# Performance work log

Measured on AMD Instinct MI355X. Metric: run time of the kernel, lower is better.

Reference implementation:

```python
import jax, jax.numpy as jnp
import numpy as np

E, D, H = 8, 512, 2048  # num_experts, features, features*mlp_ratio
B, S = 4, 512


def _lecun(key, shape):
    fan_in = shape[-2] if len(shape) >= 2 else shape[0]
    return jax.random.normal(key, shape, dtype=jnp.float32) / jnp.sqrt(jnp.float32(fan_in))


def setup_inputs() -> dict:
    key = jax.random.key(0)
    ks = jax.random.split(key, 8)
    return {
        'x_real': jax.random.normal(ks[0], (B, S, D), dtype=jnp.float32),
        'x_imag': jax.random.normal(ks[1], (B, S, D), dtype=jnp.float32),
        # gating Dense over concat([amp, phase]) -> in_features = 2*D
        'gate_W': _lecun(ks[2], (2 * D, E)),
        'gate_b': jnp.zeros((E,), jnp.float32),
        # per-expert ComplexLinear 1: D -> H
        'W1r': _lecun(ks[3], (E, D, H)),
        'W1i': _lecun(ks[4], (E, D, H)),
        'b1r': jnp.zeros((E, H), jnp.float32),
        'b1i': jnp.zeros((E, H), jnp.float32),
        # per-expert ComplexModReLU bias
        'mod_b': jnp.zeros((E, H), jnp.float32),
        # per-expert ComplexLinear 2: H -> D
        'W2r': _lecun(ks[5], (E, H, D)),
        'W2i': _lecun(ks[6], (E, H, D)),
        'b2r': jnp.zeros((E, D), jnp.float32),
        'b2i': jnp.zeros((E, D), jnp.float32),
    }


def reference(x_real, x_imag, gate_W, gate_b, W1r, W1i, b1r, b1i, mod_b, W2r, W2i, b2r, b2i):
    eps = 1e-10
    # --- gating: scores over [|z|, angle(z)] ---
    amp = jnp.sqrt(x_real ** 2 + x_imag ** 2)            # |z|, [B,S,D]
    phase = jnp.arctan2(x_imag, x_real)                  # angle(z)
    routing_input = jnp.concatenate([amp, phase], axis=-1)  # [B,S,2D]
    scores = routing_input @ gate_W + gate_b             # [B,S,E]
    probs = jax.nn.softmax(scores, axis=-1)
    idx = jnp.argmax(probs, axis=-1)                     # [B,S] top-1 expert

    # --- all experts dense (faithful to reference): complex linear 1 ---
    # (Wr + iWi)(xr + ixi) : hr = xr Wr - xi Wi ; hi = xr Wi + xi Wr
    h_r = (jnp.einsum('bsd,edh->ebsh', x_real, W1r)
           - jnp.einsum('bsd,edh->ebsh', x_imag, W1i)) + b1r[:, None, None, :]
    h_i = (jnp.einsum('bsd,edh->ebsh', x_real, W1i)
           + jnp.einsum('bsd,edh->ebsh', x_imag, W1r)) + b1i[:, None, None, :]

    # --- ComplexModReLU: relu(|z|+b) * z / (|z|+eps), |z| = sqrt(r^2+i^2+eps) ---
    a = jnp.sqrt(h_r ** 2 + h_i ** 2 + eps)              # [E,B,S,H]
    scale = jax.nn.relu(a + mod_b[:, None, None, :]) / (a + eps)
    h_r = h_r * scale
    h_i = h_i * scale

    # --- complex linear 2 ---
    o_r = (jnp.einsum('ebsh,ehd->ebsd', h_r, W2r)
           - jnp.einsum('ebsh,ehd->ebsd', h_i, W2i)) + b2r[:, None, None, :]
    o_i = (jnp.einsum('ebsh,ehd->ebsd', h_r, W2i)
           + jnp.einsum('ebsh,ehd->ebsd', h_i, W2r)) + b2i[:, None, None, :]

    # --- mask + weight (top-1): out = sum_e out_e * probs[...,e] * (argmax==e) ---
    e_ids = jnp.arange(probs.shape[-1])
    w = jnp.transpose(probs, (2, 0, 1)) * (idx[None, :, :] == e_ids[:, None, None])  # [E,B,S]
    out_r = jnp.einsum('ebs,ebsd->bsd', w, o_r)
    out_i = jnp.einsum('ebs,ebsd->bsd', w, o_i)
    return (out_r, out_i)
```

## Files before the change

kernel.cpp:

```cpp
#include <hip/hip_runtime.h>
#include <math.h>

#define NE 8
#define ND 512
#define NH 2048
#define NT 2048
#define MAXIT 40

typedef __attribute__((ext_vector_type(8))) short short8;
typedef __attribute__((ext_vector_type(4))) float f32x4;

#define GLL(g, d) __builtin_amdgcn_global_load_lds( \
    (const __attribute__((address_space(1))) void*)(g), \
    (__attribute__((address_space(3))) void*)(d), 16, 0, 0)

__device__ __forceinline__ unsigned short f2bf(float x) {
    unsigned int u = __builtin_bit_cast(unsigned int, x);
    u += 0x7FFFu + ((u >> 16) & 1u);
    return (unsigned short)(u >> 16);
}

__device__ __forceinline__ short8 lds8(const unsigned short* p) {
    return *(const short8*)p;
}

__global__ __launch_bounds__(256) void gate_kernel(
    const float* __restrict__ xr, const float* __restrict__ xi,
    const float* __restrict__ gW, const float* __restrict__ gb,
    float* __restrict__ gate_w,
    int* __restrict__ counts, int* __restrict__ tok_list,
    unsigned short* __restrict__ obr, unsigned short* __restrict__ obi)
{
    int t = blockIdx.x;
    int tid = threadIdx.x;
    const float* xrt = xr + (size_t)t * ND;
    const float* xit = xi + (size_t)t * ND;

    #pragma unroll
    for (int d = tid; d < ND; d += 256) {
        obr[(size_t)t * ND + d] = f2bf(xrt[d]);
        obi[(size_t)t * ND + d] = f2bf(xit[d]);
    }

    float acc[NE] = {0,0,0,0,0,0,0,0};
    for (int r = tid; r < 2 * ND; r += 256) {
        int d = r & (ND - 1);
        float a = xrt[d], b = xit[d];
        float v = (r < ND) ? sqrtf(a * a + b * b) : atan2f(b, a);
        const float4* g = (const float4*)(gW + (size_t)r * NE);
        float4 g0 = g[0], g1 = g[1];
        acc[0] += v * g0.x; acc[1] += v * g0.y; acc[2] += v * g0.z; acc[3] += v * g0.w;
        acc[4] += v * g1.x; acc[5] += v * g1.y; acc[6] += v * g1.z; acc[7] += v * g1.w;
    }
    #pragma unroll
    for (int e = 0; e < NE; e++) {
        for (int off = 32; off > 0; off >>= 1)
            acc[e] += __shfl_down(acc[e], off, 64);
    }
    __shared__ float part[4][NE];
    int wave = tid >> 6, lane = tid & 63;
    if (lane == 0) {
        #pragma unroll
        for (int e = 0; e < NE; e++) part[wave][e] = acc[e];
    }
    __syncthreads();
    if (tid == 0) {
        float s[NE];
        #pragma unroll
        for (int e = 0; e < NE; e++)
            s[e] = part[0][e] + part[1][e] + part[2][e] + part[3][e] + gb[e];
        int amax = 0; float m = s[0];
        #pragma unroll
        for (int e = 1; e < NE; e++) if (s[e] > m) { m = s[e]; amax = e; }
        float denom = 0.f;
        #pragma unroll
        for (int e = 0; e < NE; e++) denom += expf(s[e] - m);
        gate_w[t] = 1.0f / denom;
        int pos = atomicAdd(&counts[amax], 1);
        tok_list[amax * NT + pos] = t;
    }
}

__global__ __launch_bounds__(256) void transw_kernel(
    const float* __restrict__ s0, unsigned short* __restrict__ d0,
    const float* __restrict__ s1, unsigned short* __restrict__ d1,
    int R, int C, int* __restrict__ counts, int zero_counts)
{
    __shared__ unsigned short t[64][72];
    if (zero_counts && blockIdx.x == 0 && blockIdx.y == 0 && blockIdx.z == 0
        && threadIdx.x < 16)
        counts[threadIdx.x] = 0;
    int e = blockIdx.z;
    int c0 = blockIdx.x * 64, r0 = blockIdx.y * 64;
    size_t off = (size_t)e * R * C;
    int tid = threadIdx.x;
    #pragma unroll
    for (int p = 0; p < 2; ++p) {
        const float* src = (p ? s1 : s0) + off;
        unsigned short* dst = (p ? d1 : d0) + off;
        if (p) __syncthreads();
        #pragma unroll
        for (int i = 0; i < 4; ++i) {
            int r = i * 16 + (tid >> 4);
            int c4 = (tid & 15) * 4;
            float4 v = *(const float4*)&src[(size_t)(r0 + r) * C + c0 + c4];
            t[c4 + 0][r] = f2bf(v.x);
            t[c4 + 1][r] = f2bf(v.y);
            t[c4 + 2][r] = f2bf(v.z);
            t[c4 + 3][r] = f2bf(v.w);
        }
        __syncthreads();
        #pragma unroll
        for (int i = 0; i < 2; ++i) {
            int c = i * 32 + (tid >> 3);
            int r8 = (tid & 7) * 8;
            short8 v = *(const short8*)&t[c][r8];
            *(short8*)&dst[(size_t)(c0 + c) * R + r0 + r8] = v;
        }
    }
}


#define STAGE_(SA_R, SA_I, SB_R, SB_I, ko) do {  \
    GLL(gAr0 + (ko), SA_R + (w * 16) * 64);      \
    GLL(gAi0 + (ko), SA_I + (w * 16) * 64);      \
    GLL(gAr1 + (ko), SA_R + (w * 16 + 8) * 64);  \
    GLL(gAi1 + (ko), SA_I + (w * 16 + 8) * 64);  \
    GLL(gBr0 + (ko), SB_R + (w * 16) * 64);      \
    GLL(gBr1 + (ko), SB_R + (w * 16 + 8) * 64);  \
    GLL(gBi0 + (ko), SB_I + (w * 16) * 64);      \
    GLL(gBi1 + (ko), SB_I + (w * 16 + 8) * 64);  \
} while (0)

#define COMPUTE_(SA_R, SA_I, SB_R, SB_I) do {                                          \
    _Pragma("unroll")                                                                  \
    for (int ks = 0; ks < 2; ++ks) {                                                   \
        int pa = ((ks * 4 + quad) ^ (l15 & 7)) * 8;                                    \
        short8 br  = lds8(SB_R + (w * 16 + l15) * 64 + pa);                            \
        short8 bi2 = lds8(SB_I + (w * 16 + l15) * 64 + pa);                            \
        _Pragma("unroll")                                                              \
        for (int m = 0; m < 4; ++m) {                                                  \
            short8 ar  = lds8(SA_R + (m * 16 + l15) * 64 + pa);                        \
            short8 ai2 = lds8(SA_I + (m * 16 + l15) * 64 + pa);                        \
            aRR[m] = __builtin_amdgcn_mfma_f32_16x16x32_bf16(ar,  br,  aRR[m], 0, 0, 0); \
            aII[m] = __builtin_amdgcn_mfma_f32_16x16x32_bf16(ai2, bi2, aII[m], 0, 0, 0); \
            aRI[m] = __builtin_amdgcn_mfma_f32_16x16x32_bf16(ar,  bi2, aRI[m], 0, 0, 0); \
            aIR[m] = __builtin_amdgcn_mfma_f32_16x16x32_bf16(ai2, br,  aIR[m], 0, 0, 0); \
        }                                                                              \
    }                                                                                  \
} while (0)

#define VMW8  asm volatile("s_waitcnt vmcnt(8)" ::: "memory")
#define VMW0  asm volatile("s_waitcnt vmcnt(0)" ::: "memory")
#define BARX do {                            \
    __builtin_amdgcn_sched_barrier(0);       \
    __builtin_amdgcn_s_barrier();            \
    __builtin_amdgcn_sched_barrier(0);       \
} while (0)

#define MOE_LDS_DECL                                                        \
    __shared__ alignas(16) unsigned short sAr0[4096], sAi0[4096];           \
    __shared__ alignas(16) unsigned short sBr0[4096], sBi0[4096];           \
    __shared__ alignas(16) unsigned short sAr1[4096], sAi1[4096];           \
    __shared__ alignas(16) unsigned short sBr1[4096], sBi1[4096];

#define PIPE_LOOP(NK) do {                                                  \
    STAGE_(sAr0, sAi0, sBr0, sBi0, 0);                                      \
    VMW0; BARX;                                                             \
    _Pragma("unroll 1")                                                     \
    for (int kt = 0; kt < (NK); kt += 2) {                                  \
        if (kt + 1 < (NK)) { STAGE_(sAr1, sAi1, sBr1, sBi1, (kt + 1) * 64); VMW8; } \
        else VMW0;                                                          \
        BARX;                                                               \
        __builtin_amdgcn_s_setprio(1);                                      \
        COMPUTE_(sAr0, sAi0, sBr0, sBi0);                                   \
        __builtin_amdgcn_s_setprio(0);                                      \
        BARX;                                                               \
        if (kt + 2 < (NK)) { STAGE_(sAr0, sAi0, sBr0, sBi0, (kt + 2) * 64); VMW8; } \
        else VMW0;                                                          \
        BARX;                                                               \
        __builtin_amdgcn_s_setprio(1);                                      \
        COMPUTE_(sAr1, sAi1, sBr1, sBi1);                                   \
        __builtin_amdgcn_s_setprio(0);                                      \
        BARX;                                                               \
    }                                                                       \
} while (0)

__device__ __forceinline__ bool find_item(const int* counts, int item,
                                          int& e, int& mt, int& n) {
    int rem = item;
    for (e = 0; e < NE; ++e) {
        n = counts[e];
        int m = (n + 63) >> 6;
        if (rem < m) { mt = rem; return true; }
        rem -= m;
    }
    return false;
}

__global__ __launch_bounds__(256, 2) void moe1_kernel(
    const unsigned short* __restrict__ xbr, const unsigned short* __restrict__ xbi,
    const unsigned short* __restrict__ w1tr, const unsigned short* __restrict__ w1ti,
    const float* __restrict__ b1r, const float* __restrict__ b1i,
    const float* __restrict__ mod_b,
    const int* __restrict__ counts, const int* __restrict__ tok_list,
    unsigned short* __restrict__ hr, unsigned short* __restrict__ hi)
{
    int e, mt, n;
    if (!find_item(counts, blockIdx.x >> 5, e, mt, n)) return;
    int nt = blockIdx.x & 31;
    int mbase = mt * 64, n0 = nt * 64;

    int tid = threadIdx.x;
    int w = tid >> 6, l = tid & 63;
    int l15 = l & 15, quad = l >> 4;
    int swz = (((l & 7) ^ ((l >> 3) & 7)) * 8);

    MOE_LDS_DECL

    const int* tl = tok_list + e * NT;
    int ia0 = mbase + w * 16 + (l >> 3);
    int ia1 = ia0 + 8;
    int ra0 = tl[ia0 < n ? ia0 : n - 1];
    int ra1 = tl[ia1 < n ? ia1 : n - 1];
    const unsigned short* gAr0 = xbr + (size_t)ra0 * ND + swz;
    const unsigned short* gAi0 = xbi + (size_t)ra0 * ND + swz;
    const unsigned short* gAr1 = xbr + (size_t)ra1 * ND + swz;
    const unsigned short* gAi1 = xbi + (size_t)ra1 * ND + swz;
    size_t brow = (size_t)e * NH + n0 + w * 16 + (l >> 3);
    const unsigned short* gBr0 = w1tr + brow * ND + swz;
    const unsigned short* gBr1 = w1tr + (brow + 8) * ND + swz;
    const unsigned short* gBi0 = w1ti + brow * ND + swz;
    const unsigned short* gBi1 = w1ti + (brow + 8) * ND + swz;

    f32x4 aRR[4] = {}, aII[4] = {}, aRI[4] = {}, aIR[4] = {};

    PIPE_LOOP(ND / 64);

    int col = n0 + w * 16 + l15;
    float bre = b1r[(size_t)e * NH + col];
    float bie = b1i[(size_t)e * NH + col];
    float mbv = mod_b[(size_t)e * NH + col];
    #pragma unroll
    for (int m = 0; m < 4; ++m) {
        #pragma unroll
        for (int r = 0; r < 4; ++r) {
            int tix = m * 16 + quad * 4 + r;
            if (mbase + tix >= n) continue;
            int tok = tl[mbase + tix];
            float vr = aRR[m][r] - aII[m][r] + bre;
            float vi = aRI[m][r] + aIR[m][r] + bie;
            float a = sqrtf(vr * vr + vi * vi + 1e-10f);
            float sc = fmaxf(a + mbv, 0.0f) / (a + 1e-10f);
            hr[(size_t)tok * NH + col] = f2bf(vr * sc);
            hi[(size_t)tok * NH + col] = f2bf(vi * sc);
        }
    }
}

__global__ __launch_bounds__(256, 2) void moe2_kernel(
    const unsigned short* __restrict__ hr, const unsigned short* __restrict__ hi,
    const unsigned short* __restrict__ w2tr, const unsigned short* __restrict__ w2ti,
    const float* __restrict__ b2r, const float* __restrict__ b2i,
    const int* __restrict__ counts, const int* __restrict__ tok_list,
    const float* __restrict__ gate_w,
    float* __restrict__ out)
{
    int e, mt, n;
    if (!find_item(counts, blockIdx.x >> 3, e, mt, n)) return;
    int nt = blockIdx.x & 7;
    int mbase = mt * 64, n0 = nt * 64;

    int tid = threadIdx.x;
    int w = tid >> 6, l = tid & 63;
    int l15 = l & 15, quad = l >> 4;
    int swz = (((l & 7) ^ ((l >> 3) & 7)) * 8);

    MOE_LDS_DECL

    const int* tl = tok_list + e * NT;
    int ia0 = mbase + w * 16 + (l >> 3);
    int ia1 = ia0 + 8;
    int ra0 = tl[ia0 < n ? ia0 : n - 1];
    int ra1 = tl[ia1 < n ? ia1 : n - 1];
    const unsigned short* gAr0 = hr + (size_t)ra0 * NH + swz;
    const unsigned short* gAi0 = hi + (size_t)ra0 * NH + swz;
    const unsigned short* gAr1 = hr + (size_t)ra1 * NH + swz;
    const unsigned short* gAi1 = hi + (size_t)ra1 * NH + swz;
    size_t brow = (size_t)e * ND + n0 + w * 16 + (l >> 3);
    const unsigned short* gBr0 = w2tr + brow * NH + swz;
    const unsigned short* gBr1 = w2tr + (brow + 8) * NH + swz;
    const unsigned short* gBi0 = w2ti + brow * NH + swz;
    const unsigned short* gBi1 = w2ti + (brow + 8) * NH + swz;

    f32x4 aRR[4] = {}, aII[4] = {}, aRI[4] = {}, aIR[4] = {};

    PIPE_LOOP(NH / 64);

    int col = n0 + w * 16 + l15;
    float bre = b2r[(size_t)e * ND + col];
    float bie = b2i[(size_t)e * ND + col];
    #pragma unroll
    for (int m = 0; m < 4; ++m) {
        #pragma unroll
        for (int r = 0; r < 4; ++r) {
            int tix = m * 16 + quad * 4 + r;
            if (mbase + tix >= n) continue;
            int tok = tl[mbase + tix];
            float gw = gate_w[tok];
            out[(size_t)tok * ND + col] = (aRR[m][r] - aII[m][r] + bre) * gw;
            out[(size_t)NT * ND + (size_t)tok * ND + col] = (aRI[m][r] + aIR[m][r] + bie) * gw;
        }
    }
}

extern "C" void kernel_launch(void* const* d_in, const int* in_sizes, int n_in,
                              void* d_out, int out_size, void* d_ws, size_t ws_size,
                              hipStream_t stream) {
    const float* xr   = (const float*)d_in[0];
    const float* xi   = (const float*)d_in[1];
    const float* gW   = (const float*)d_in[2];
    const float* gb   = (const float*)d_in[3];
    const float* W1r  = (const float*)d_in[4];
    const float* W1i  = (const float*)d_in[5];
    const float* b1r  = (const float*)d_in[6];
    const float* b1i  = (const float*)d_in[7];
    const float* modb = (const float*)d_in[8];
    const float* W2r  = (const float*)d_in[9];
    const float* W2i  = (const float*)d_in[10];
    const float* b2r  = (const float*)d_in[11];
    const float* b2i  = (const float*)d_in[12];
    float* out = (float*)d_out;

    char* ws = (char*)d_ws;
    int*   counts   = (int*)ws;
    float* gate_w   = (float*)(ws + 256);
    int*   tok_list = (int*)(ws + 256 + 8192);
    size_t off = 256 + 8192 + (size_t)NE * NT * 4;
    unsigned short* xbr  = (unsigned short*)(ws + off); off += (size_t)NT * ND * 2;
    unsigned short* xbi  = (unsigned short*)(ws + off); off += (size_t)NT * ND * 2;
    unsigned short* w1tr = (unsigned short*)(ws + off); off += (size_t)NE * ND * NH * 2;
    unsigned short* w1ti = (unsigned short*)(ws + off); off += (size_t)NE * ND * NH * 2;
    unsigned short* w2tr = (unsigned short*)(ws + off); off += (size_t)NE * ND * NH * 2;
    unsigned short* w2ti = (unsigned short*)(ws + off); off += (size_t)NE * ND * NH * 2;
    unsigned short* h_r  = (unsigned short*)(ws + off); off += (size_t)NT * NH * 2;
    unsigned short* h_i  = (unsigned short*)(ws + off); off += (size_t)NT * NH * 2;

    transw_kernel<<<dim3(NH / 64, ND / 64, NE), 256, 0, stream>>>(
        W1r, w1tr, W1i, w1ti, ND, NH, counts, 1);
    transw_kernel<<<dim3(ND / 64, NH / 64, NE), 256, 0, stream>>>(
        W2r, w2tr, W2i, w2ti, NH, ND, counts, 0);
    gate_kernel<<<NT, 256, 0, stream>>>(xr, xi, gW, gb, gate_w, counts, tok_list, xbr, xbi);
    moe1_kernel<<<MAXIT * 32, 256, 0, stream>>>(
        xbr, xbi, w1tr, w1ti, b1r, b1i, modb, counts, tok_list, h_r, h_i);
    moe2_kernel<<<MAXIT * 8, 256, 0, stream>>>(
        h_r, h_i, w2tr, w2ti, b2r, b2i, counts, tok_list, gate_w, out);
}
```

Measured before the change: 297.6 us.

## Use 4-stage LDS ring pipeline, merge weight transposes, remap block-to-tile order

```diff
diff --git a/kernel.cpp b/kernel.cpp
--- a/kernel.cpp
+++ b/kernel.cpp
@@ -82,16 +82,25 @@
 }
 
 __global__ __launch_bounds__(256) void transw_kernel(
-    const float* __restrict__ s0, unsigned short* __restrict__ d0,
-    const float* __restrict__ s1, unsigned short* __restrict__ d1,
-    int R, int C, int* __restrict__ counts, int zero_counts)
+    const float* __restrict__ W1r, unsigned short* __restrict__ w1tr,
+    const float* __restrict__ W1i, unsigned short* __restrict__ w1ti,
+    const float* __restrict__ W2r, unsigned short* __restrict__ w2tr,
+    const float* __restrict__ W2i, unsigned short* __restrict__ w2ti,
+    int* __restrict__ counts)
 {
-    __shared__ unsigned short t[64][72];
-    if (zero_counts && blockIdx.x == 0 && blockIdx.y == 0 && blockIdx.z == 0
-        && threadIdx.x < 16)
+    __shared__ unsigned short tile[64][72];
+    int z = blockIdx.z;
+    int e = z & 7, which = z >> 3;
+    if (z == 0 && blockIdx.x == 0 && blockIdx.y == 0 && threadIdx.x < 16)
         counts[threadIdx.x] = 0;
-    int e = blockIdx.z;
-    int c0 = blockIdx.x * 64, r0 = blockIdx.y * 64;
+    int R = which ? NH : ND;
+    int C = which ? ND : NH;
+    int c0 = (which ? blockIdx.y : blockIdx.x) * 64;
+    int r0 = (which ? blockIdx.x : blockIdx.y) * 64;
+    const float* s0 = which ? W2r : W1r;
+    const float* s1 = which ? W2i : W1i;
+    unsigned short* d0 = which ? w2tr : w1tr;
+    unsigned short* d1 = which ? w2ti : w1ti;
     size_t off = (size_t)e * R * C;
     int tid = threadIdx.x;
     #pragma unroll
@@ -104,86 +113,78 @@
             int r = i * 16 + (tid >> 4);
             int c4 = (tid & 15) * 4;
             float4 v = *(const float4*)&src[(size_t)(r0 + r) * C + c0 + c4];
-            t[c4 + 0][r] = f2bf(v.x);
-            t[c4 + 1][r] = f2bf(v.y);
-            t[c4 + 2][r] = f2bf(v.z);
-            t[c4 + 3][r] = f2bf(v.w);
+            tile[c4 + 0][r] = f2bf(v.x);
+            tile[c4 + 1][r] = f2bf(v.y);
+            tile[c4 + 2][r] = f2bf(v.z);
+            tile[c4 + 3][r] = f2bf(v.w);
         }
         __syncthreads();
         #pragma unroll
         for (int i = 0; i < 2; ++i) {
             int c = i * 32 + (tid >> 3);
             int r8 = (tid & 7) * 8;
-            short8 v = *(const short8*)&t[c][r8];
+            short8 v = *(const short8*)&tile[c][r8];
             *(short8*)&dst[(size_t)(c0 + c) * R + r0 + r8] = v;
         }
     }
 }
 
 
-#define STAGE_(SA_R, SA_I, SB_R, SB_I, ko) do {  \
-    GLL(gAr0 + (ko), SA_R + (w * 16) * 64);      \
-    GLL(gAi0 + (ko), SA_I + (w * 16) * 64);      \
-    GLL(gAr1 + (ko), SA_R + (w * 16 + 8) * 64);  \
-    GLL(gAi1 + (ko), SA_I + (w * 16 + 8) * 64);  \
-    GLL(gBr0 + (ko), SB_R + (w * 16) * 64);      \
-    GLL(gBr1 + (ko), SB_R + (w * 16 + 8) * 64);  \
-    GLL(gBi0 + (ko), SB_I + (w * 16) * 64);      \
-    GLL(gBi1 + (ko), SB_I + (w * 16 + 8) * 64);  \
-} while (0)
-
-#define COMPUTE_(SA_R, SA_I, SB_R, SB_I) do {                                          \
-    _Pragma("unroll")                                                                  \
-    for (int ks = 0; ks < 2; ++ks) {                                                   \
-        int pa = ((ks * 4 + quad) ^ (l15 & 7)) * 8;                                    \
-        short8 br  = lds8(SB_R + (w * 16 + l15) * 64 + pa);                            \
-        short8 bi2 = lds8(SB_I + (w * 16 + l15) * 64 + pa);                            \
-        _Pragma("unroll")                                                              \
-        for (int m = 0; m < 4; ++m) {                                                  \
-            short8 ar  = lds8(SA_R + (m * 16 + l15) * 64 + pa);                        \
-            short8 ai2 = lds8(SA_I + (m * 16 + l15) * 64 + pa);                        \
-            aRR[m] = __builtin_amdgcn_mfma_f32_16x16x32_bf16(ar,  br,  aRR[m], 0, 0, 0); \
-            aII[m] = __builtin_amdgcn_mfma_f32_16x16x32_bf16(ai2, bi2, aII[m], 0, 0, 0); \
-            aRI[m] = __builtin_amdgcn_mfma_f32_16x16x32_bf16(ar,  bi2, aRI[m], 0, 0, 0); \
-            aIR[m] = __builtin_amdgcn_mfma_f32_16x16x32_bf16(ai2, br,  aIR[m], 0, 0, 0); \
-        }                                                                              \
-    }                                                                                  \
-} while (0)
-
-#define VMW8  asm volatile("s_waitcnt vmcnt(8)" ::: "memory")
-#define VMW0  asm volatile("s_waitcnt vmcnt(0)" ::: "memory")
+#define VMW16 asm volatile("s_waitcnt vmcnt(16)" ::: "memory")
+#define VMW8  asm volatile("s_waitcnt vmcnt(8)"  ::: "memory")
+#define VMW0  asm volatile("s_waitcnt vmcnt(0)"  ::: "memory")
 #define BARX do {                            \
     __builtin_amdgcn_sched_barrier(0);       \
     __builtin_amdgcn_s_barrier();            \
     __builtin_amdgcn_sched_barrier(0);       \
 } while (0)
-
-#define MOE_LDS_DECL                                                        \
-    __shared__ alignas(16) unsigned short sAr0[4096], sAi0[4096];           \
-    __shared__ alignas(16) unsigned short sBr0[4096], sBi0[4096];           \
-    __shared__ alignas(16) unsigned short sAr1[4096], sAi1[4096];           \
-    __shared__ alignas(16) unsigned short sBr1[4096], sBi1[4096];
-
-#define PIPE_LOOP(NK) do {                                                  \
-    STAGE_(sAr0, sAi0, sBr0, sBi0, 0);                                      \
-    VMW0; BARX;                                                             \
-    _Pragma("unroll 1")                                                     \
-    for (int kt = 0; kt < (NK); kt += 2) {                                  \
-        if (kt + 1 < (NK)) { STAGE_(sAr1, sAi1, sBr1, sBi1, (kt + 1) * 64); VMW8; } \
-        else VMW0;                                                          \
-        BARX;                                                               \
-        __builtin_amdgcn_s_setprio(1);                                      \
-        COMPUTE_(sAr0, sAi0, sBr0, sBi0);                                   \
-        __builtin_amdgcn_s_setprio(0);                                      \
-        BARX;                                                               \
-        if (kt + 2 < (NK)) { STAGE_(sAr0, sAi0, sBr0, sBi0, (kt + 2) * 64); VMW8; } \
-        else VMW0;                                                          \
-        BARX;                                                               \
-        __builtin_amdgcn_s_setprio(1);                                      \
-        COMPUTE_(sAr1, sAi1, sBr1, sBi1);                                   \
-        __builtin_amdgcn_s_setprio(0);                                      \
-        BARX;                                                               \
-    }                                                                       \
+#define SP1 __builtin_amdgcn_s_setprio(1)
+#define SP0 __builtin_amdgcn_s_setprio(0)
+
+#define RING_DECL __shared__ alignas(16) unsigned short ring[4][16384];
+
+#define STAGE_S(s, ko) do {                                  \
+    unsigned short* _b = &ring[s][0];                        \
+    GLL(gAr0 + (ko), _b + (w * 16) * 64);                    \
+    GLL(gAr1 + (ko), _b + (w * 16 + 8) * 64);                \
+    GLL(gAi0 + (ko), _b + 4096 + (w * 16) * 64);             \
+    GLL(gAi1 + (ko), _b + 4096 + (w * 16 + 8) * 64);         \
+    GLL(gBr0 + (ko), _b + 8192 + (w * 16) * 64);             \
+    GLL(gBr1 + (ko), _b + 8192 + (w * 16 + 8) * 64);         \
+    GLL(gBi0 + (ko), _b + 12288 + (w * 16) * 64);            \
+    GLL(gBi1 + (ko), _b + 12288 + (w * 16 + 8) * 64);        \
+} while (0)
+
+#define COMPUTE_S(s) do {                                                        \
+    const unsigned short* _sa = &ring[s][0];                                     \
+    _Pragma("unroll")                                                            \
+    for (int ks = 0; ks < 2; ++ks) {                                             \
+        int pa = ((ks * 4 + quad) ^ (l15 & 7)) * 8;                              \
+        short8 br  = lds8(_sa + 8192  + (w * 16 + l15) * 64 + pa);               \
+        short8 bi2 = lds8(_sa + 12288 + (w * 16 + l15) * 64 + pa);               \
+        _Pragma("unroll")                                                        \
+        for (int m = 0; m < 4; ++m) {                                            \
+            short8 ar  = lds8(_sa + (m * 16 + l15) * 64 + pa);                   \
+            short8 ai2 = lds8(_sa + 4096 + (m * 16 + l15) * 64 + pa);            \
+            aRR[m] = __builtin_amdgcn_mfma_f32_16x16x32_bf16(ar,  br,  aRR[m], 0, 0, 0); \
+            aII[m] = __builtin_amdgcn_mfma_f32_16x16x32_bf16(ai2, bi2, aII[m], 0, 0, 0); \
+            aRI[m] = __builtin_amdgcn_mfma_f32_16x16x32_bf16(ar,  bi2, aRI[m], 0, 0, 0); \
+            aIR[m] = __builtin_amdgcn_mfma_f32_16x16x32_bf16(ai2, br,  aIR[m], 0, 0, 0); \
+        }                                                                        \
+    }                                                                            \
+} while (0)
+
+#define PIPE_RING(NK) do {                                                   \
+    STAGE_S(0, 0); STAGE_S(1, 64); STAGE_S(2, 128);                          \
+    _Pragma("unroll 1")                                                      \
+    for (int t = 0; t < (NK) - 3; ++t) {                                     \
+        VMW16; BARX;                                                         \
+        STAGE_S((t + 3) & 3, (t + 3) * 64);                                  \
+        SP1; COMPUTE_S(t & 3); SP0;                                          \
+    }                                                                        \
+    VMW16; BARX; SP1; COMPUTE_S(((NK) - 3) & 3); SP0;                        \
+    VMW8;  BARX; SP1; COMPUTE_S(((NK) - 2) & 3); SP0;                        \
+    VMW0;  BARX; SP1; COMPUTE_S(((NK) - 1) & 3); SP0;                        \
 } while (0)
 
 __device__ __forceinline__ bool find_item(const int* counts, int item,
@@ -198,7 +199,7 @@
     return false;
 }
 
-__global__ __launch_bounds__(256, 2) void moe1_kernel(
+__global__ __launch_bounds__(256, 1) void moe1_kernel(
     const unsigned short* __restrict__ xbr, const unsigned short* __restrict__ xbi,
     const unsigned short* __restrict__ w1tr, const unsigned short* __restrict__ w1ti,
     const float* __restrict__ b1r, const float* __restrict__ b1i,
@@ -206,9 +207,12 @@
     const int* __restrict__ counts, const int* __restrict__ tok_list,
     unsigned short* __restrict__ hr, unsigned short* __restrict__ hi)
 {
+    int bid = blockIdx.x;
+    int xg = bid & 7, tg = bid >> 3;
+    int nt = tg & 31;
+    int item = (tg >> 5) * 8 + xg;
     int e, mt, n;
-    if (!find_item(counts, blockIdx.x >> 5, e, mt, n)) return;
-    int nt = blockIdx.x & 31;
+    if (!find_item(counts, item, e, mt, n)) return;
     int mbase = mt * 64, n0 = nt * 64;
 
     int tid = threadIdx.x;
@@ -216,7 +220,7 @@
     int l15 = l & 15, quad = l >> 4;
     int swz = (((l & 7) ^ ((l >> 3) & 7)) * 8);
 
-    MOE_LDS_DECL
+    RING_DECL
 
     const int* tl = tok_list + e * NT;
     int ia0 = mbase + w * 16 + (l >> 3);
@@ -235,7 +239,7 @@
 
     f32x4 aRR[4] = {}, aII[4] = {}, aRI[4] = {}, aIR[4] = {};
 
-    PIPE_LOOP(ND / 64);
+    PIPE_RING(ND / 64);
 
     int col = n0 + w * 16 + l15;
     float bre = b1r[(size_t)e * NH + col];
@@ -258,7 +262,7 @@
     }
 }
 
-__global__ __launch_bounds__(256, 2) void moe2_kernel(
+__global__ __launch_bounds__(256, 1) void moe2_kernel(
     const unsigned short* __restrict__ hr, const unsigned short* __restrict__ hi,
     const unsigned short* __restrict__ w2tr, const unsigned short* __restrict__ w2ti,
     const float* __restrict__ b2r, const float* __restrict__ b2i,
@@ -266,9 +270,12 @@
     const float* __restrict__ gate_w,
     float* __restrict__ out)
 {
+    int bid = blockIdx.x;
+    int xg = bid & 7, tg = bid >> 3;
+    int nt = tg & 7;
+    int item = (tg >> 3) * 8 + xg;
     int e, mt, n;
-    if (!find_item(counts, blockIdx.x >> 3, e, mt, n)) return;
-    int nt = blockIdx.x & 7;
+    if (!find_item(counts, item, e, mt, n)) return;
     int mbase = mt * 64, n0 = nt * 64;
 
     int tid = threadIdx.x;
@@ -276,7 +283,7 @@
     int l15 = l & 15, quad = l >> 4;
     int swz = (((l & 7) ^ ((l >> 3) & 7)) * 8);
 
-    MOE_LDS_DECL
+    RING_DECL
 
     const int* tl = tok_list + e * NT;
     int ia0 = mbase + w * 16 + (l >> 3);
@@ -295,7 +302,7 @@
 
     f32x4 aRR[4] = {}, aII[4] = {}, aRI[4] = {}, aIR[4] = {};
 
-    PIPE_LOOP(NH / 64);
+    PIPE_RING(NH / 64);
 
     int col = n0 + w * 16 + l15;
     float bre = b2r[(size_t)e * ND + col];
@@ -346,13 +353,11 @@
     unsigned short* h_r  = (unsigned short*)(ws + off); off += (size_t)NT * NH * 2;
     unsigned short* h_i  = (unsigned short*)(ws + off); off += (size_t)NT * NH * 2;
 
-    transw_kernel<<<dim3(NH / 64, ND / 64, NE), 256, 0, stream>>>(
-        W1r, w1tr, W1i, w1ti, ND, NH, counts, 1);
-    transw_kernel<<<dim3(ND / 64, NH / 64, NE), 256, 0, stream>>>(
-        W2r, w2tr, W2i, w2ti, NH, ND, counts, 0);
+    transw_kernel<<<dim3(32, 8, 16), 256, 0, stream>>>(
+        W1r, w1tr, W1i, w1ti, W2r, w2tr, W2i, w2ti, counts);
     gate_kernel<<<NT, 256, 0, stream>>>(xr, xi, gW, gb, gate_w, counts, tok_list, xbr, xbi);
-    moe1_kernel<<<MAXIT * 32, 256, 0, stream>>>(
+    moe1_kernel<<<8 * 32 * (MAXIT / 8), 256, 0, stream>>>(
         xbr, xbi, w1tr, w1ti, b1r, b1i, modb, counts, tok_list, h_r, h_i);
-    moe2_kernel<<<MAXIT * 8, 256, 0, stream>>>(
+    moe2_kernel<<<8 * 8 * (MAXIT / 8), 256, 0, stream>>>(
         h_r, h_i, w2tr, w2ti, b2r, b2i, counts, tok_list, gate_w, out);
 }
```

After: 336.4 us. +13.0%, slower.
